# Kernel tuning notes

Measured on AMD Instinct MI355X. Metric: run time of the kernel, lower is better.

Reference implementation:

```python
import jax, jax.numpy as jnp
import numpy as np


def setup_inputs() -> dict:
    key = jax.random.key(0)
    kq, kk, kv, km = jax.random.split(key, 4)
    B, H, S, D = 2, 16, 2048, 64
    Q = jax.random.normal(kq, (B, H, S, D), dtype=jnp.float32)
    K = jax.random.normal(kk, (B, H, S, D), dtype=jnp.float32)
    V = jax.random.normal(kv, (B, H, S, D), dtype=jnp.float32)
    attn_mask = jax.random.randint(km, (B, 1, S, S), 0, 2).astype(jnp.bool_)
    return {"Q": Q, "K": K, "V": V, "attn_mask": attn_mask}


def reference(Q, K, V, attn_mask):
    d_k = Q.shape[-1]
    # scores = Q @ K^T / sqrt(d_k)  -> [B, H, S, S]
    scores = jnp.einsum('bhqd,bhkd->bhqk', Q, K) / jnp.sqrt(jnp.float32(d_k))
    # faithful to torch masked_fill_(attn_mask, 1e-9): masked positions set to 1e-9
    scores = jnp.where(attn_mask, jnp.float32(1e-9), scores)
    attn = jax.nn.softmax(scores, axis=-1)
    context = jnp.einsum('bhqk,bhkd->bhqd', attn, V)
    return (context, attn)
```

## Files before the change

### kernel.cpp

```cpp
#include <hip/hip_runtime.h>

#define BB 2
#define HH 16
#define SS 2048
#define DD 64
#define QR 8

typedef __attribute__((ext_vector_type(8))) _Float16 half8;
typedef __attribute__((ext_vector_type(4))) _Float16 half4;
typedef __attribute__((ext_vector_type(4))) float f32x4;
typedef __attribute__((ext_vector_type(4))) unsigned int u32x4;

__device__ __forceinline__ half8 cvt8(f32x4 a, f32x4 b) {
  half8 r;
  r[0] = (_Float16)a[0]; r[1] = (_Float16)a[1];
  r[2] = (_Float16)a[2]; r[3] = (_Float16)a[3];
  r[4] = (_Float16)b[0]; r[5] = (_Float16)b[1];
  r[6] = (_Float16)b[2]; r[7] = (_Float16)b[3];
  return r;
}

__global__ __launch_bounds__(256, 8)
void cvt_kv(const float* __restrict__ K, const float* __restrict__ V,
            _Float16* __restrict__ K16, _Float16* __restrict__ V16) {
  const size_t N4 = (size_t)BB * HH * SS * DD / 4;
  for (size_t i = (size_t)blockIdx.x * blockDim.x + threadIdx.x; i < N4;
       i += (size_t)gridDim.x * blockDim.x) {
    f32x4 k = *((const f32x4*)K + i);
    f32x4 v = *((const f32x4*)V + i);
    half4 kh, vh;
#pragma unroll
    for (int j = 0; j < 4; ++j) { kh[j] = (_Float16)k[j]; vh[j] = (_Float16)v[j]; }
    *((half4*)K16 + i) = kh;
    *((half4*)V16 + i) = vh;
  }
}

template <bool F16>
__global__ __launch_bounds__(512, 8)
void sdpa_kernel(const float* __restrict__ Q, const float* __restrict__ K,
                 const float* __restrict__ V, const void* __restrict__ M,
                 const _Float16* __restrict__ K16g, const _Float16* __restrict__ V16g,
                 float* __restrict__ out_ctx, float* __restrict__ out_attn) {
  __shared__ _Float16 E[QR * 2048];
  __shared__ unsigned int mbits[QR][68];
  __shared__ float zacc[8][QR];
  __shared__ f32x4 pscr[4][64];

  const int bh   = blockIdx.y;
  const int b    = bh >> 4;
  const int q0   = blockIdx.x * QR;
  const int tid  = threadIdx.x;
  const int wave = tid >> 6;
  const int lane = tid & 63;
  const int col  = lane & 15;
  const int quad = lane >> 4;

  const unsigned int* mw = (const unsigned int*)M;
  unsigned int probe = mw[lane];
  unsigned long long bi = __ballot(probe <= 1u);
  unsigned long long bf = __ballot(probe == 0u || probe == 0x3f800000u);
  const int mmode = (bi == ~0ull) ? 0 : ((bf == ~0ull) ? 1 : 2);

  const float* Qb = Q + (size_t)bh * SS * DD;
  const float* Kb = K + (size_t)bh * SS * DD;
  const float* Vb = V + (size_t)bh * SS * DD;
  const _Float16* K16b = K16g + (size_t)bh * SS * DD;
  const _Float16* V16b = V16g + (size_t)bh * SS * DD;

  half8 aQ0, aQ1;
  {
    const float* qp = Qb + (size_t)(q0 + (col & 7)) * DD + quad * 8;
    f32x4 x0 = *(const f32x4*)(qp);
    f32x4 x1 = *(const f32x4*)(qp + 4);
    f32x4 x2 = *(const f32x4*)(qp + 32);
    f32x4 x3 = *(const f32x4*)(qp + 36);
    aQ0 = cvt8(x0, x1);
    aQ1 = cvt8(x2, x3);
  }

  {
    unsigned int* mflat = &mbits[0][0];
    for (int i = tid; i < QR * 68; i += 512) mflat[i] = 0u;
    __syncthreads();
    if (mmode == 2) {
      const unsigned char* mb = (const unsigned char*)M + (size_t)b * SS * SS + (size_t)q0 * SS;
#pragma unroll
      for (int j = 0; j < 2; ++j) {
        const int lin = (tid + j * 512) * 16;
        u32x4 v = *(const u32x4*)(mb + lin);
        unsigned int bits = 0;
#pragma unroll
        for (int w = 0; w < 4; ++w) {
          unsigned int x = v[w];
          bits |= ((x & 0x000000ffu) ? 1u : 0u) << (w * 4 + 0);
          bits |= ((x & 0x0000ff00u) ? 1u : 0u) << (w * 4 + 1);
          bits |= ((x & 0x00ff0000u) ? 1u : 0u) << (w * 4 + 2);
          bits |= ((x & 0xff000000u) ? 1u : 0u) << (w * 4 + 3);
        }
        const int row = lin >> 11, key0 = lin & 2047;
        atomicOr(&mbits[row][key0 >> 5], bits << (key0 & 31));
      }
    } else {
      const unsigned int* mv4 = (const unsigned int*)M + (size_t)b * SS * SS + (size_t)q0 * SS;
#pragma unroll
      for (int j = 0; j < 8; ++j) {
        const int lin = (tid + j * 512) * 4;
        u32x4 v = *(const u32x4*)(mv4 + lin);
        unsigned int bits = 0;
        bits |= v[0] ? 1u : 0u;
        bits |= v[1] ? 2u : 0u;
        bits |= v[2] ? 4u : 0u;
        bits |= v[3] ? 8u : 0u;
        const int row = lin >> 11, key0 = lin & 2047;
        atomicOr(&mbits[row][key0 >> 5], bits << (key0 & 31));
      }
    }
    __syncthreads();
  }

  float zpart[4] = {0.f, 0.f, 0.f, 0.f};
#pragma unroll 2
  for (int n0 = wave * 16; n0 < SS; n0 += 128) {
    half8 bK0, bK1;
    if (F16) {
      const _Float16* kp = K16b + (size_t)(n0 + col) * DD + quad * 8;
      bK0 = *(const half8*)(kp);
      bK1 = *(const half8*)(kp + 32);
    } else {
      const float* kp = Kb + (size_t)(n0 + col) * DD + quad * 8;
      f32x4 x0 = *(const f32x4*)(kp);
      f32x4 x1 = *(const f32x4*)(kp + 4);
      f32x4 x2 = *(const f32x4*)(kp + 32);
      f32x4 x3 = *(const f32x4*)(kp + 36);
      bK0 = cvt8(x0, x1);
      bK1 = cvt8(x2, x3);
    }
    f32x4 c = {0.f, 0.f, 0.f, 0.f};
    c = __builtin_amdgcn_mfma_f32_16x16x32_f16(aQ0, bK0, c, 0, 0, 0);
    c = __builtin_amdgcn_mfma_f32_16x16x32_f16(aQ1, bK1, c, 0, 0, 0);
    const int key    = n0 + col;
    const int mword  = n0 >> 5;
    const int mshift = (n0 & 16) + col;
    if (quad < 2) {
#pragma unroll
      for (int r = 0; r < 4; ++r) {
        const int row = quad * 4 + r;
        const int mv = (mbits[row][mword] >> mshift) & 1;
        const float sc = mv ? 1e-9f : c[r] * 0.125f;
        const float e  = __expf(sc);
        zpart[r] += e;
        const int gp = (key >> 3) ^ row;
        E[row * 2048 + gp * 8 + (key & 7)] = (_Float16)e;
      }
    }
  }
#pragma unroll
  for (int r = 0; r < 4; ++r) {
    float z = zpart[r];
    z += __shfl_xor(z, 1, 64);
    z += __shfl_xor(z, 2, 64);
    z += __shfl_xor(z, 4, 64);
    z += __shfl_xor(z, 8, 64);
    if (quad < 2 && col == 0) zacc[wave][quad * 4 + r] = z;
  }
  __syncthreads();

  const int d0 = (wave & 3) << 4;
  const int h  = wave >> 2;
  const int kbase = h << 10;
  float rz;
  {
    float z = 0.f;
#pragma unroll
    for (int w = 0; w < 8; ++w) z += zacc[w][wave];
    rz = 1.0f / z;
  }
  f32x4 u = {0.f, 0.f, 0.f, 0.f};
#pragma unroll 4
  for (int t = 0; t < 32; ++t) {
    const int kk0 = kbase + t * 32;
    const int gp = ((kk0 + quad * 8) >> 3) ^ (col & 7);
    half8 aP = *(const half8*)&E[(col & 7) * 2048 + gp * 8];
    half8 bV;
    if (F16) {
      const _Float16* vp = V16b + (size_t)(kk0 + quad * 8) * DD + d0 + col;
#pragma unroll
      for (int jj = 0; jj < 8; ++jj) bV[jj] = vp[(size_t)jj * DD];
    } else {
      const float* vp = Vb + (size_t)(kk0 + quad * 8) * DD + d0 + col;
#pragma unroll
      for (int jj = 0; jj < 8; ++jj) bV[jj] = (_Float16)vp[(size_t)jj * DD];
    }
    u = __builtin_amdgcn_mfma_f32_16x16x32_f16(aP, bV, u, 0, 0, 0);
    if ((t & 7) == 7) {
      const int i   = t >> 3;
      const int row = wave;
      const int gpr = i * 64 + lane;
      half8 v = *(const half8*)&E[row * 2048 + gpr * 8];
      const int gcol = i * 64 + (lane ^ row);
      float* arow = out_attn + ((size_t)bh * SS + (q0 + row)) * SS;
      f32x4 w0, w1;
#pragma unroll
      for (int j = 0; j < 4; ++j) {
        w0[j] = (float)v[j] * rz;
        w1[j] = (float)v[j + 4] * rz;
      }
      *(f32x4*)(arow + gcol * 8)     = w0;
      *(f32x4*)(arow + gcol * 8 + 4) = w1;
    }
  }
  if (h) pscr[wave & 3][lane] = u;
  __syncthreads();

  if (h == 0) {
    f32x4 u2 = pscr[wave][lane];
    if (quad < 2) {
#pragma unroll
      for (int r = 0; r < 4; ++r) {
        const int row = quad * 4 + r;
        float z = 0.f;
#pragma unroll
        for (int w = 0; w < 8; ++w) z += zacc[w][row];
        out_ctx[((size_t)bh * SS + (q0 + row)) * DD + d0 + col] = (u[r] + u2[r]) / z;
      }
    }
  }
}

extern "C" void kernel_launch(void* const* d_in, const int* in_sizes, int n_in,
                              void* d_out, int out_size, void* d_ws, size_t ws_size,
                              hipStream_t stream) {
  const float* Q = (const float*)d_in[0];
  const float* K = (const float*)d_in[1];
  const float* V = (const float*)d_in[2];
  const void*  M = d_in[3];
  float* ctx  = (float*)d_out;
  float* attn = ctx + (size_t)BB * HH * SS * DD;
  dim3 grid(SS / QR, BB * HH);
  const size_t nkv = (size_t)BB * HH * SS * DD;
  if (ws_size >= 2 * nkv * sizeof(_Float16) && d_ws != nullptr) {
    _Float16* K16 = (_Float16*)d_ws;
    _Float16* V16 = K16 + nkv;
    cvt_kv<<<dim3(2048), 256, 0, stream>>>(K, V, K16, V16);
    sdpa_kernel<true><<<grid, 512, 0, stream>>>(Q, K, V, M, K16, V16, ctx, attn);
  } else {
    sdpa_kernel<false><<<grid, 512, 0, stream>>>(Q, K, V, M, nullptr, nullptr, ctx, attn);
  }
}
```

Before: 964.0 us.

## Store fp16 V transposed so PV MFMA loads one vector per lane

The conversion kernel now writes V in fp16 in a [D][S] transposed layout, going through a shared-memory tile, while K stays row-major. The PV loop in the attention kernel then fetches each MFMA B operand as one contiguous half8 load instead of eight strided 2-byte gathers. The loop is also split into four groups of eight steps, with the attention-row write-out after each group. The cost is a slightly more complex conversion kernel with an LDS transpose and a barrier.

```diff
diff --git a/kernel.cpp b/kernel.cpp
--- a/kernel.cpp
+++ b/kernel.cpp
@@ -22,17 +22,32 @@
 
 __global__ __launch_bounds__(256, 8)
 void cvt_kv(const float* __restrict__ K, const float* __restrict__ V,
-            _Float16* __restrict__ K16, _Float16* __restrict__ V16) {
-  const size_t N4 = (size_t)BB * HH * SS * DD / 4;
-  for (size_t i = (size_t)blockIdx.x * blockDim.x + threadIdx.x; i < N4;
-       i += (size_t)gridDim.x * blockDim.x) {
-    f32x4 k = *((const f32x4*)K + i);
-    f32x4 v = *((const f32x4*)V + i);
-    half4 kh, vh;
-#pragma unroll
-    for (int j = 0; j < 4; ++j) { kh[j] = (_Float16)k[j]; vh[j] = (_Float16)v[j]; }
-    *((half4*)K16 + i) = kh;
-    *((half4*)V16 + i) = vh;
+            _Float16* __restrict__ K16, _Float16* __restrict__ V16T) {
+  __shared__ _Float16 T[64][80];
+  const int bh = blockIdx.x >> 5;
+  const int kt = blockIdx.x & 31;
+  const int tid = threadIdx.x;
+  const float* Kb = K + ((size_t)bh * SS + kt * 64) * DD;
+  const float* Vb = V + ((size_t)bh * SS + kt * 64) * DD;
+  _Float16* K16b = K16 + ((size_t)bh * SS + kt * 64) * DD;
+#pragma unroll
+  for (int i = 0; i < 4; ++i) {
+    const int lin = (tid + i * 256) * 4;
+    const int r = lin >> 6, d = lin & 63;
+    f32x4 kx = *(const f32x4*)(Kb + lin);
+    f32x4 vx = *(const f32x4*)(Vb + lin);
+    half4 kh;
+#pragma unroll
+    for (int j = 0; j < 4; ++j) { kh[j] = (_Float16)kx[j]; T[d + j][r] = (_Float16)vx[j]; }
+    *(half4*)(K16b + lin) = kh;
+  }
+  __syncthreads();
+#pragma unroll
+  for (int i = 0; i < 2; ++i) {
+    const int lin = (tid + i * 256) * 8;
+    const int d = lin >> 6, kq = lin & 63;
+    half8 v = *(const half8*)&T[d][kq];
+    *(half8*)(V16T + ((size_t)bh * DD + d) * SS + kt * 64 + kq) = v;
   }
 }
 
@@ -40,7 +55,7 @@
 __global__ __launch_bounds__(512, 8)
 void sdpa_kernel(const float* __restrict__ Q, const float* __restrict__ K,
                  const float* __restrict__ V, const void* __restrict__ M,
-                 const _Float16* __restrict__ K16g, const _Float16* __restrict__ V16g,
+                 const _Float16* __restrict__ K16g, const _Float16* __restrict__ V16Tg,
                  float* __restrict__ out_ctx, float* __restrict__ out_attn) {
   __shared__ _Float16 E[QR * 2048];
   __shared__ unsigned int mbits[QR][68];
@@ -65,8 +80,8 @@
   const float* Qb = Q + (size_t)bh * SS * DD;
   const float* Kb = K + (size_t)bh * SS * DD;
   const float* Vb = V + (size_t)bh * SS * DD;
-  const _Float16* K16b = K16g + (size_t)bh * SS * DD;
-  const _Float16* V16b = V16g + (size_t)bh * SS * DD;
+  const _Float16* K16b  = K16g  + (size_t)bh * SS * DD;
+  const _Float16* V16Tb = V16Tg + (size_t)bh * DD * SS;
 
   half8 aQ0, aQ1;
   {
@@ -176,25 +191,28 @@
     for (int w = 0; w < 8; ++w) z += zacc[w][wave];
     rz = 1.0f / z;
   }
+  const int klocal = quad * 8;
+  const _Float16* vrow = F16 ? (V16Tb + (size_t)(d0 + col) * SS + kbase + klocal) : nullptr;
   f32x4 u = {0.f, 0.f, 0.f, 0.f};
-#pragma unroll 4
-  for (int t = 0; t < 32; ++t) {
-    const int kk0 = kbase + t * 32;
-    const int gp = ((kk0 + quad * 8) >> 3) ^ (col & 7);
-    half8 aP = *(const half8*)&E[(col & 7) * 2048 + gp * 8];
-    half8 bV;
-    if (F16) {
-      const _Float16* vp = V16b + (size_t)(kk0 + quad * 8) * DD + d0 + col;
-#pragma unroll
-      for (int jj = 0; jj < 8; ++jj) bV[jj] = vp[(size_t)jj * DD];
-    } else {
-      const float* vp = Vb + (size_t)(kk0 + quad * 8) * DD + d0 + col;
-#pragma unroll
-      for (int jj = 0; jj < 8; ++jj) bV[jj] = (_Float16)vp[(size_t)jj * DD];
-    }
-    u = __builtin_amdgcn_mfma_f32_16x16x32_f16(aP, bV, u, 0, 0, 0);
-    if ((t & 7) == 7) {
-      const int i   = t >> 3;
+  for (int tt = 0; tt < 4; ++tt) {
+#pragma unroll
+    for (int s = 0; s < 8; ++s) {
+      const int t = tt * 8 + s;
+      const int kk0 = kbase + t * 32;
+      const int gp = ((kk0 + klocal) >> 3) ^ (col & 7);
+      half8 aP = *(const half8*)&E[(col & 7) * 2048 + gp * 8];
+      half8 bV;
+      if (F16) {
+        bV = *(const half8*)(vrow + t * 32);
+      } else {
+        const float* vp = Vb + (size_t)(kk0 + klocal) * DD + d0 + col;
+#pragma unroll
+        for (int jj = 0; jj < 8; ++jj) bV[jj] = (_Float16)vp[(size_t)jj * DD];
+      }
+      u = __builtin_amdgcn_mfma_f32_16x16x32_f16(aP, bV, u, 0, 0, 0);
+    }
+    {
+      const int i   = tt;
       const int row = wave;
       const int gpr = i * 64 + lane;
       half8 v = *(const half8*)&E[row * 2048 + gpr * 8];
@@ -240,10 +258,10 @@
   dim3 grid(SS / QR, BB * HH);
   const size_t nkv = (size_t)BB * HH * SS * DD;
   if (ws_size >= 2 * nkv * sizeof(_Float16) && d_ws != nullptr) {
-    _Float16* K16 = (_Float16*)d_ws;
-    _Float16* V16 = K16 + nkv;
-    cvt_kv<<<dim3(2048), 256, 0, stream>>>(K, V, K16, V16);
-    sdpa_kernel<true><<<grid, 512, 0, stream>>>(Q, K, V, M, K16, V16, ctx, attn);
+    _Float16* K16  = (_Float16*)d_ws;
+    _Float16* V16T = K16 + nkv;
+    cvt_kv<<<dim3(BB * HH * 32), 256, 0, stream>>>(K, V, K16, V16T);
+    sdpa_kernel<true><<<grid, 512, 0, stream>>>(Q, K, V, M, K16, V16T, ctx, attn);
   } else {
     sdpa_kernel<false><<<grid, 512, 0, stream>>>(Q, K, V, M, nullptr, nullptr, ctx, attn);
   }
```

Measured after the change: 1.030 ms. 6.8% more time.

## Remap blocks to spread heads across XCDs and prefetch next K tile

Applied to the files above, without the earlier changes.

Flattens the grid and remaps block index so that consecutive blocks (dispatched round-robin across the XCDs) map to different (b,h) slices. Each XCD then repeatedly works on the same few heads, which should improve L2 reuse of K/V. Also software-pipelines the K fp16 loads in the score loop by prefetching the next tile into registers and drops the unroll pragma. The prefetch raises register pressure.

```diff
diff --git a/kernel.cpp b/kernel.cpp
--- a/kernel.cpp
+++ b/kernel.cpp
@@ -47,9 +47,10 @@
   __shared__ float zacc[8][QR];
   __shared__ f32x4 pscr[4][64];
 
-  const int bh   = blockIdx.y;
+  const int flat = blockIdx.x;
+  const int bh   = ((flat & 7) << 2) | ((flat >> 3) & 3);
+  const int q0   = (flat >> 5) * QR;
   const int b    = bh >> 4;
-  const int q0   = blockIdx.x * QR;
   const int tid  = threadIdx.x;
   const int wave = tid >> 6;
   const int lane = tid & 63;
@@ -120,19 +121,28 @@
   }
 
   float zpart[4] = {0.f, 0.f, 0.f, 0.f};
-#pragma unroll 2
+  const _Float16* kp = F16 ? (K16b + (size_t)(wave * 16 + col) * DD + quad * 8) : nullptr;
+  half8 cK0, cK1;
+  if (F16) {
+    cK0 = *(const half8*)(kp);
+    cK1 = *(const half8*)(kp + 32);
+  }
   for (int n0 = wave * 16; n0 < SS; n0 += 128) {
     half8 bK0, bK1;
     if (F16) {
-      const _Float16* kp = K16b + (size_t)(n0 + col) * DD + quad * 8;
-      bK0 = *(const half8*)(kp);
-      bK1 = *(const half8*)(kp + 32);
+      bK0 = cK0;
+      bK1 = cK1;
+      if (n0 + 128 < SS) {
+        kp += 128 * DD;
+        cK0 = *(const half8*)(kp);
+        cK1 = *(const half8*)(kp + 32);
+      }
     } else {
-      const float* kp = Kb + (size_t)(n0 + col) * DD + quad * 8;
-      f32x4 x0 = *(const f32x4*)(kp);
-      f32x4 x1 = *(const f32x4*)(kp + 4);
-      f32x4 x2 = *(const f32x4*)(kp + 32);
-      f32x4 x3 = *(const f32x4*)(kp + 36);
+      const float* kf = Kb + (size_t)(n0 + col) * DD + quad * 8;
+      f32x4 x0 = *(const f32x4*)(kf);
+      f32x4 x1 = *(const f32x4*)(kf + 4);
+      f32x4 x2 = *(const f32x4*)(kf + 32);
+      f32x4 x3 = *(const f32x4*)(kf + 36);
       bK0 = cvt8(x0, x1);
       bK1 = cvt8(x2, x3);
     }
@@ -176,19 +186,20 @@
     for (int w = 0; w < 8; ++w) z += zacc[w][wave];
     rz = 1.0f / z;
   }
+  const int klocal = quad * 8;
   f32x4 u = {0.f, 0.f, 0.f, 0.f};
 #pragma unroll 4
   for (int t = 0; t < 32; ++t) {
     const int kk0 = kbase + t * 32;
-    const int gp = ((kk0 + quad * 8) >> 3) ^ (col & 7);
+    const int gp = ((kk0 + klocal) >> 3) ^ (col & 7);
     half8 aP = *(const half8*)&E[(col & 7) * 2048 + gp * 8];
     half8 bV;
     if (F16) {
-      const _Float16* vp = V16b + (size_t)(kk0 + quad * 8) * DD + d0 + col;
+      const _Float16* vp = V16b + (size_t)(kk0 + klocal) * DD + d0 + col;
 #pragma unroll
       for (int jj = 0; jj < 8; ++jj) bV[jj] = vp[(size_t)jj * DD];
     } else {
-      const float* vp = Vb + (size_t)(kk0 + quad * 8) * DD + d0 + col;
+      const float* vp = Vb + (size_t)(kk0 + klocal) * DD + d0 + col;
 #pragma unroll
       for (int jj = 0; jj < 8; ++jj) bV[jj] = (_Float16)vp[(size_t)jj * DD];
     }
@@ -237,7 +248,7 @@
   const void*  M = d_in[3];
   float* ctx  = (float*)d_out;
   float* attn = ctx + (size_t)BB * HH * SS * DD;
-  dim3 grid(SS / QR, BB * HH);
+  dim3 grid(BB * HH * (SS / QR));
   const size_t nkv = (size_t)BB * HH * SS * DD;
   if (ws_size >= 2 * nkv * sizeof(_Float16) && d_ws != nullptr) {
     _Float16* K16 = (_Float16*)d_ws;
```

New measurement: 950.3 us. Within noise of the previous version (-1.4%).
